# Optimization experiments

Measured on AMD Instinct MI355X. Metric: run time of the kernel, lower is better.

## Reference

```python
import math
import jax, jax.numpy as jnp
import numpy as np

R_MIN, R_MAX, R_BINS = 0.0, 10.0, 64
Z_MIN, Z_MAX, Z_BINS = -2.0, 2.0, 64
DR = (R_MAX - R_MIN) / R_BINS
DZ = (Z_MAX - Z_MIN) / Z_BINS
N = 16777216


def setup_inputs() -> dict:
    key = jax.random.key(0)
    k1, k2 = jax.random.split(key)
    positions = jax.random.normal(k1, (N, 3), dtype=jnp.float32)
    masses = jax.random.uniform(k2, (N,), dtype=jnp.float32)
    return {"positions": positions, "masses": masses}


def _volume():
    redge = R_MIN + jnp.arange(R_BINS + 1, dtype=jnp.float32) * DR
    area = math.pi * (redge[1:] ** 2 - redge[:-1] ** 2)  # [R_BINS]
    return area * DZ


def reference(positions, masses):
    r_cyl = jnp.sqrt(positions[:, 0] ** 2 + positions[:, 1] ** 2)
    i = jnp.floor((r_cyl - R_MIN) / DR).astype(jnp.int32)
    j = jnp.floor((positions[:, 2] - Z_MIN) / DZ).astype(jnp.int32)
    gd = (i >= 0) & (i < R_BINS) & (j >= 0) & (j < Z_BINS)
    flat = jnp.where(gd, i * Z_BINS + j, 0)
    w = jnp.where(gd, masses, 0.0)
    mass_in_bin = jnp.zeros((R_BINS * Z_BINS,), dtype=masses.dtype).at[flat].add(w)
    mass_in_bin = mass_in_bin.reshape(R_BINS, Z_BINS)
    surface_density = mass_in_bin / _volume()[:, None]
    return surface_density
```

## Files before the change

kernel.cpp:

```cpp
#include <hip/hip_runtime.h>
#include <math.h>

#define R_BINS 64
#define Z_BINS 64
#define NBINS (R_BINS * Z_BINS)
#define BLOCK 512
#define WAVES_PER_BLOCK 8
#define GRID 1024

static constexpr float DR     = 10.0f / 64.0f;
static constexpr float DZ     = 4.0f  / 64.0f;
static constexpr float INV_DR = 6.4f;
static constexpr float INV_DZ = 16.0f;

__global__ __launch_bounds__(BLOCK) void hist_kernel(const float4* __restrict__ pos4,
                                                     const float* __restrict__ mass,
                                                     float* __restrict__ gbins,
                                                     int nchunks) {
    __shared__ float lbins[NBINS];
    __shared__ float4 stage[WAVES_PER_BLOCK][192];

    const int lane = threadIdx.x & 63;
    const int w    = threadIdx.x >> 6;

    for (int b = threadIdx.x; b < NBINS; b += BLOCK) lbins[b] = 0.0f;
    __syncthreads();

    const int totalWaves = gridDim.x * WAVES_PER_BLOCK;
    float* s = (float*)&stage[w][0];

    for (int c = blockIdx.x * WAVES_PER_BLOCK + w; c < nchunks; c += totalWaves) {
        const float4* pb = pos4 + (size_t)192 * c;
        const float4 f0 = pb[lane];
        const float4 f1 = pb[64 + lane];
        const float4 f2 = pb[128 + lane];

        const float* mb = mass + (size_t)256 * c;
        const float m0 = mb[lane];
        const float m1 = mb[64 + lane];
        const float m2 = mb[128 + lane];
        const float m3 = mb[192 + lane];

        stage[w][lane]       = f0;
        stage[w][64 + lane]  = f1;
        stage[w][128 + lane] = f2;
        __asm__ volatile("s_waitcnt lgkmcnt(0)" ::: "memory");
        __builtin_amdgcn_wave_barrier();

        const float ms[4] = {m0, m1, m2, m3};
#pragma unroll
        for (int k = 0; k < 4; ++k) {
            const int p = 64 * k + lane;
            const float x = s[3 * p];
            const float y = s[3 * p + 1];
            const float z = s[3 * p + 2];
            const float r = sqrtf(x * x + y * y);
            const int i = (int)(r * INV_DR);
            const int j = (int)floorf((z + 2.0f) * INV_DZ);
            if (i < R_BINS && (unsigned)j < (unsigned)Z_BINS) {
                atomicAdd(&lbins[i * Z_BINS + j], ms[k]);
            }
        }
        __asm__ volatile("" ::: "memory");
        __builtin_amdgcn_wave_barrier();
    }

    __syncthreads();
    for (int b = threadIdx.x; b < NBINS; b += BLOCK) {
        const float v = lbins[b];
        if (v != 0.0f) atomicAdd(&gbins[b], v);
    }
}

__global__ void tail_kernel(const float* __restrict__ pos,
                            const float* __restrict__ mass,
                            float* __restrict__ gbins,
                            int start, int n) {
    const int t = start + blockIdx.x * blockDim.x + threadIdx.x;
    if (t < n) {
        const float x = pos[3 * t], y = pos[3 * t + 1], z = pos[3 * t + 2];
        const float r = sqrtf(x * x + y * y);
        const int i = (int)(r * INV_DR);
        const int j = (int)floorf((z + 2.0f) * INV_DZ);
        if (i < R_BINS && (unsigned)j < (unsigned)Z_BINS) {
            atomicAdd(&gbins[i * Z_BINS + j], mass[t]);
        }
    }
}

__global__ __launch_bounds__(256) void finalize_kernel(const float* __restrict__ gbins,
                                                       float* __restrict__ out) {
    const int idx = blockIdx.x * blockDim.x + threadIdx.x;
    if (idx < NBINS) {
        const int i = idx / Z_BINS;
        const float r0 = (float)i * DR;
        const float r1 = (float)(i + 1) * DR;
        const float area = (float)M_PI * (r1 * r1 - r0 * r0);
        out[idx] = gbins[idx] / (area * DZ);
    }
}

extern "C" void kernel_launch(void* const* d_in, const int* in_sizes, int n_in,
                              void* d_out, int out_size, void* d_ws, size_t ws_size,
                              hipStream_t stream) {
    const float* positions = (const float*)d_in[0];
    const float* masses    = (const float*)d_in[1];
    float* out   = (float*)d_out;
    float* gbins = (float*)d_ws;

    const int n = in_sizes[1];
    const int nchunks = n / 256;
    const int rem = n - nchunks * 256;

    hipMemsetAsync(gbins, 0, NBINS * sizeof(float), stream);

    hist_kernel<<<GRID, BLOCK, 0, stream>>>((const float4*)positions, masses,
                                            gbins, nchunks);
    if (rem > 0) {
        tail_kernel<<<(rem + 255) / 256, 256, 0, stream>>>(positions, masses,
                                                           gbins, nchunks * 256, n);
    }
    finalize_kernel<<<(NBINS + 255) / 256, 256, 0, stream>>>(gbins, out);
}
```

Before: 327.6 us.

## Load 8 particles per thread with float4 and spread global flush over slabs

Each thread now loads eight consecutive particles directly as six float4 position loads and two float4 mass loads, replacing the per-wave LDS staging transpose. The grid goes to 2048 blocks of 256 threads. Each block's final flush goes into one of 64 global slabs instead of a single histogram, cutting contention on the global atomics. A combined reduce-finalize kernel then sums the slabs. In exchange, the per-thread loads are strided rather than lane-coalesced, and a larger workspace memset is needed.

```diff
diff --git a/kernel.cpp b/kernel.cpp
--- a/kernel.cpp
+++ b/kernel.cpp
@@ -4,77 +4,66 @@
 #define R_BINS 64
 #define Z_BINS 64
 #define NBINS (R_BINS * Z_BINS)
-#define BLOCK 512
-#define WAVES_PER_BLOCK 8
-#define GRID 1024
+#define BLOCK 256
+#define GRID 2048
+#define NSLAB 64
 
 static constexpr float DR     = 10.0f / 64.0f;
 static constexpr float DZ     = 4.0f  / 64.0f;
 static constexpr float INV_DR = 6.4f;
 static constexpr float INV_DZ = 16.0f;
 
+__device__ __forceinline__ void bin_one(float x, float y, float z, float m,
+                                        float* lbins) {
+    const float r = sqrtf(x * x + y * y);
+    const int i = (int)(r * INV_DR);
+    const int j = (int)floorf((z + 2.0f) * INV_DZ);
+    if (i < R_BINS && (unsigned)j < (unsigned)Z_BINS) {
+        atomicAdd(&lbins[i * Z_BINS + j], m);
+    }
+}
+
 __global__ __launch_bounds__(BLOCK) void hist_kernel(const float4* __restrict__ pos4,
-                                                     const float* __restrict__ mass,
-                                                     float* __restrict__ gbins,
-                                                     int nchunks) {
+                                                     const float4* __restrict__ mass4,
+                                                     float* __restrict__ slabs,
+                                                     int n8) {
     __shared__ float lbins[NBINS];
-    __shared__ float4 stage[WAVES_PER_BLOCK][192];
-
-    const int lane = threadIdx.x & 63;
-    const int w    = threadIdx.x >> 6;
-
     for (int b = threadIdx.x; b < NBINS; b += BLOCK) lbins[b] = 0.0f;
     __syncthreads();
 
-    const int totalWaves = gridDim.x * WAVES_PER_BLOCK;
-    float* s = (float*)&stage[w][0];
+    const int stride = gridDim.x * BLOCK;
+    for (int q = blockIdx.x * BLOCK + threadIdx.x; q < n8; q += stride) {
+        const float4* pb = pos4 + (size_t)6 * q;
+        const float4 p0 = pb[0];
+        const float4 p1 = pb[1];
+        const float4 p2 = pb[2];
+        const float4 p3 = pb[3];
+        const float4 p4 = pb[4];
+        const float4 p5 = pb[5];
+        const float4 ma = mass4[2 * q];
+        const float4 mb = mass4[2 * q + 1];
 
-    for (int c = blockIdx.x * WAVES_PER_BLOCK + w; c < nchunks; c += totalWaves) {
-        const float4* pb = pos4 + (size_t)192 * c;
-        const float4 f0 = pb[lane];
-        const float4 f1 = pb[64 + lane];
-        const float4 f2 = pb[128 + lane];
-
-        const float* mb = mass + (size_t)256 * c;
-        const float m0 = mb[lane];
-        const float m1 = mb[64 + lane];
-        const float m2 = mb[128 + lane];
-        const float m3 = mb[192 + lane];
-
-        stage[w][lane]       = f0;
-        stage[w][64 + lane]  = f1;
-        stage[w][128 + lane] = f2;
-        __asm__ volatile("s_waitcnt lgkmcnt(0)" ::: "memory");
-        __builtin_amdgcn_wave_barrier();
-
-        const float ms[4] = {m0, m1, m2, m3};
-#pragma unroll
-        for (int k = 0; k < 4; ++k) {
-            const int p = 64 * k + lane;
-            const float x = s[3 * p];
-            const float y = s[3 * p + 1];
-            const float z = s[3 * p + 2];
-            const float r = sqrtf(x * x + y * y);
-            const int i = (int)(r * INV_DR);
-            const int j = (int)floorf((z + 2.0f) * INV_DZ);
-            if (i < R_BINS && (unsigned)j < (unsigned)Z_BINS) {
-                atomicAdd(&lbins[i * Z_BINS + j], ms[k]);
-            }
-        }
-        __asm__ volatile("" ::: "memory");
-        __builtin_amdgcn_wave_barrier();
+        bin_one(p0.x, p0.y, p0.z, ma.x, lbins);
+        bin_one(p0.w, p1.x, p1.y, ma.y, lbins);
+        bin_one(p1.z, p1.w, p2.x, ma.z, lbins);
+        bin_one(p2.y, p2.z, p2.w, ma.w, lbins);
+        bin_one(p3.x, p3.y, p3.z, mb.x, lbins);
+        bin_one(p3.w, p4.x, p4.y, mb.y, lbins);
+        bin_one(p4.z, p4.w, p5.x, mb.z, lbins);
+        bin_one(p5.y, p5.z, p5.w, mb.w, lbins);
     }
 
     __syncthreads();
+    float* slab = slabs + (size_t)(blockIdx.x % NSLAB) * NBINS;
     for (int b = threadIdx.x; b < NBINS; b += BLOCK) {
         const float v = lbins[b];
-        if (v != 0.0f) atomicAdd(&gbins[b], v);
+        if (v != 0.0f) atomicAdd(&slab[b], v);
     }
 }
 
 __global__ void tail_kernel(const float* __restrict__ pos,
                             const float* __restrict__ mass,
-                            float* __restrict__ gbins,
+                            float* __restrict__ slabs,
                             int start, int n) {
     const int t = start + blockIdx.x * blockDim.x + threadIdx.x;
     if (t < n) {
@@ -83,20 +72,23 @@
         const int i = (int)(r * INV_DR);
         const int j = (int)floorf((z + 2.0f) * INV_DZ);
         if (i < R_BINS && (unsigned)j < (unsigned)Z_BINS) {
-            atomicAdd(&gbins[i * Z_BINS + j], mass[t]);
+            atomicAdd(&slabs[i * Z_BINS + j], mass[t]);
         }
     }
 }
 
-__global__ __launch_bounds__(256) void finalize_kernel(const float* __restrict__ gbins,
-                                                       float* __restrict__ out) {
+__global__ __launch_bounds__(256) void reduce_finalize_kernel(
+        const float* __restrict__ slabs, float* __restrict__ out) {
     const int idx = blockIdx.x * blockDim.x + threadIdx.x;
     if (idx < NBINS) {
+        float s = 0.0f;
+#pragma unroll 8
+        for (int k = 0; k < NSLAB; ++k) s += slabs[(size_t)k * NBINS + idx];
         const int i = idx / Z_BINS;
         const float r0 = (float)i * DR;
         const float r1 = (float)(i + 1) * DR;
         const float area = (float)M_PI * (r1 * r1 - r0 * r0);
-        out[idx] = gbins[idx] / (area * DZ);
+        out[idx] = s / (area * DZ);
     }
 }
 
@@ -106,19 +98,19 @@
     const float* positions = (const float*)d_in[0];
     const float* masses    = (const float*)d_in[1];
     float* out   = (float*)d_out;
-    float* gbins = (float*)d_ws;
+    float* slabs = (float*)d_ws;
 
     const int n = in_sizes[1];
-    const int nchunks = n / 256;
-    const int rem = n - nchunks * 256;
+    const int n8 = n / 8;
+    const int rem = n - n8 * 8;
 
-    hipMemsetAsync(gbins, 0, NBINS * sizeof(float), stream);
+    hipMemsetAsync(slabs, 0, (size_t)NSLAB * NBINS * sizeof(float), stream);
 
-    hist_kernel<<<GRID, BLOCK, 0, stream>>>((const float4*)positions, masses,
-                                            gbins, nchunks);
+    hist_kernel<<<GRID, BLOCK, 0, stream>>>((const float4*)positions,
+                                            (const float4*)masses, slabs, n8);
     if (rem > 0) {
         tail_kernel<<<(rem + 255) / 256, 256, 0, stream>>>(positions, masses,
-                                                           gbins, nchunks * 256, n);
+                                                           slabs, n8 * 8, n);
     }
-    finalize_kernel<<<(NBINS + 255) / 256, 256, 0, stream>>>(gbins, out);
+    reduce_finalize_kernel<<<(NBINS + 255) / 256, 256, 0, stream>>>(slabs, out);
 }
```

Result: no change. 329.1 us (+0.4%).
